# Optimization experiments

Hardware: AMD Instinct MI355X
Metric: run time of the kernel (lower is better)

Reference implementation:

```python
import math
import jax, jax.numpy as jnp
import numpy as np

NUM_HEADS = 16
HEAD_DIM = 128
BLOCK = 256
EPS = 1e-6


def _get_slopes(n):
    def p2(n):
        start = 2 ** (-2 ** (-(math.log2(n) - 3)))
        return [start * start ** i for i in range(n)]
    if math.log2(n).is_integer():
        return p2(n)
    c = 2 ** math.floor(math.log2(n))
    return p2(c) + _get_slopes(2 * c)[0::2][: n - c]


def setup_inputs() -> dict:
    key = jax.random.key(0)
    ks = jax.random.split(key, 4)
    d_in, d_out = 2048, 2048
    x = jax.random.normal(ks[0], (2, 4096, d_in), dtype=jnp.float32)
    Wqkv = jax.random.normal(ks[1], (d_in, 3 * NUM_HEADS * HEAD_DIM), dtype=jnp.float32) * 0.02
    Wg = jax.random.normal(ks[2], (d_in, NUM_HEADS * HEAD_DIM), dtype=jnp.float32) * 0.02
    Wout = jax.random.normal(ks[3], (NUM_HEADS * HEAD_DIM, d_out), dtype=jnp.float32) * 0.02
    norm_w = jnp.ones((NUM_HEADS * HEAD_DIM,), dtype=jnp.float32)
    return {"x": x, "Wqkv": Wqkv, "Wg": Wg, "Wout": Wout, "norm_w": norm_w}


def reference(x, Wqkv, Wg, Wout, norm_w):
    b, n, _ = x.shape
    h, d = NUM_HEADS, HEAD_DIM
    nb = n // BLOCK  # seq_len chosen divisible by block_size

    # slopes (ALiBi-style), shape [h,1,1]
    slope = jnp.asarray(_get_slopes(h), dtype=jnp.float32).reshape(h, 1, 1)

    qkv = jax.nn.silu(x @ Wqkv)                       # [b,n,3hd]
    qkv = qkv.reshape(b, n, h, 3 * d)
    q, k, v = jnp.split(qkv, 3, axis=-1)              # each [b,n,h,d]
    q = q.transpose(0, 2, 1, 3)                       # [b,h,n,d]
    k = k.transpose(0, 2, 1, 3)
    v = v.transpose(0, 2, 1, 3)

    # per-position decay factors within a block
    arr = jnp.arange(BLOCK, dtype=jnp.float32) + 1.0          # [B]
    q_decay = jnp.exp(-slope * arr[:, None])                  # [h,B,1]
    k_decay = jnp.exp(-slope * (BLOCK - arr[:, None]))        # [h,B,1]
    idx = arr[:, None] - arr[None, :]                         # [B,B]
    diag_decay = jnp.where(idx >= 0, jnp.exp(-slope[None] * idx[None, None]), 0.0)  # [1,h,B,B]
    block_decay = jnp.exp(-slope * BLOCK)                     # [h,1,1]

    # blocked xs: [nb, b, h, B, d]
    def to_blocks(t):
        return t.reshape(b, h, nb, BLOCK, d).transpose(2, 0, 1, 3, 4)

    qb, kb, vb = to_blocks(q), to_blocks(k), to_blocks(v)

    def step(kv, blk):
        qi, ki, vi = blk                                       # [b,h,B,d]
        # inter-block: (qi * q_decay) @ kv  -> [b,h,B,d]
        non_diag = jnp.einsum('bhmd,bhde->bhme', qi * q_decay, kv)
        # intra-block causal decayed attention
        qk = jnp.einsum('bhmd,bhnd->bhmn', qi, ki) * diag_decay
        diag = jnp.einsum('bhmn,bhne->bhme', qk, vi)
        out = non_diag + diag
        kv_new = block_decay * kv + jnp.einsum('bhmd,bhme->bhde', ki * k_decay, vi)
        return kv_new, out

    kv0 = jnp.zeros((b, h, d, d), dtype=jnp.float32)
    _, out_blocks = jax.lax.scan(step, kv0, (qb, kb, vb))      # [nb,b,h,B,d]
    o = out_blocks.transpose(1, 2, 0, 3, 4).reshape(b, h, n, d)
    o = o.transpose(0, 2, 1, 3).reshape(b, n, h * d)           # [b,n,hd]

    # T5 (RMS) LayerNorm
    var = jnp.mean(o * o, axis=-1, keepdims=True)
    o = o * jax.lax.rsqrt(var + EPS) * norm_w

    # output gate and projection
    o = jax.nn.sigmoid(x @ Wg) * o
    return o @ Wout
```

## Files before the change

kernel.cpp:

```cpp
#include <hip/hip_runtime.h>
#include <cstddef>

typedef float f32x4 __attribute__((ext_vector_type(4)));
typedef __bf16 bf16x8 __attribute__((ext_vector_type(8)));
typedef unsigned short u16x8 __attribute__((ext_vector_type(8)));
typedef unsigned short u16x4 __attribute__((ext_vector_type(4)));

constexpr int NB = 2, S = 4096, H = 16, D = 128;
constexpr int DIN = 2048, NQKV = 6144, HD = 2048;
constexpr int BLK = 256, NBL = 16;

constexpr size_t SZ_XB    = (size_t)NB * S * DIN * 2;
constexpr size_t SZ_WQKVT = (size_t)NQKV * DIN * 2;
constexpr size_t SZ_WGT   = (size_t)HD * DIN * 2;
constexpr size_t SZ_WOUTT = (size_t)HD * HD * 2;
constexpr size_t SZ_QKVB  = (size_t)NB * S * NQKV * 2;
constexpr size_t SZ_GB    = (size_t)NB * S * HD * 2;
constexpr size_t SZ_ST    = (size_t)NB * H * NBL * D * D * 2;
constexpr size_t SZ_OB    = (size_t)NB * S * HD * 2;

__device__ __forceinline__ float bf2f(unsigned short u) {
  return __uint_as_float(((unsigned)u) << 16);
}
__device__ __forceinline__ unsigned short f2bf(float f) {
  unsigned u = __float_as_uint(f);
  u += 0x7fffu + ((u >> 16) & 1u);
  return (unsigned short)(u >> 16);
}
__device__ __forceinline__ void gload16(const void* g, void* l) {
  __builtin_amdgcn_global_load_lds(
      (const __attribute__((address_space(1))) unsigned int*)g,
      (__attribute__((address_space(3))) unsigned int*)l, 16, 0, 0);
}

__global__ __launch_bounds__(256) void cvt_bf16(
    const float* __restrict__ in, unsigned short* __restrict__ out) {
  const size_t id = (size_t)blockIdx.x * 256 + threadIdx.x;
  const float4 a = *(const float4*)&in[id * 8];
  const float4 c = *(const float4*)&in[id * 8 + 4];
  u16x8 o;
  o[0] = f2bf(a.x); o[1] = f2bf(a.y); o[2] = f2bf(a.z); o[3] = f2bf(a.w);
  o[4] = f2bf(c.x); o[5] = f2bf(c.y); o[6] = f2bf(c.z); o[7] = f2bf(c.w);
  *(u16x8*)&out[id * 8] = o;
}

__global__ __launch_bounds__(256) void transpose_cvt(
    const float* __restrict__ W, unsigned short* __restrict__ Wt, int K, int N) {
  __shared__ unsigned short tile[32][33];
  const int n0 = blockIdx.x * 32, k0 = blockIdx.y * 32;
  const int t = threadIdx.x;
  const int r = t >> 3, c4 = (t & 7) * 4;
  const float4 v = *(const float4*)&W[(size_t)(k0 + r) * N + n0 + c4];
  tile[r][c4 + 0] = f2bf(v.x);
  tile[r][c4 + 1] = f2bf(v.y);
  tile[r][c4 + 2] = f2bf(v.z);
  tile[r][c4 + 3] = f2bf(v.w);
  __syncthreads();
  u16x4 o;
  #pragma unroll
  for (int i = 0; i < 4; ++i) o[i] = tile[c4 + i][r];
  *(u16x4*)&Wt[(size_t)(n0 + r) * K + k0 + c4] = o;
}

template<int ACT>
__global__ __launch_bounds__(512, 2) void gemm256(
    const unsigned short* __restrict__ A, const unsigned short* __restrict__ Bt,
    void* __restrict__ C, int M, int N, int K) {
  __shared__ unsigned short lds[65536];
  char* ldsb = (char*)lds;
  const int t = threadIdx.x;
  const int lane = t & 63, wave = t >> 6;
  const int wr = wave >> 2, wc = wave & 3;

  const int nbn = N >> 8;
  const int nwg = gridDim.x;
  int lin = blockIdx.x;
  lin = (lin & 7) * (nwg >> 3) + (lin >> 3);
  const int bm = lin / nbn, bn = lin % nbn;

  const int subr = lane >> 2;
  const int sw = (subr & 6) << 3;
  const int cstg = ((((lane & 3) << 4) ^ sw) >> 1);
  const int r0 = wave * 32 + subr;
  const unsigned short* srcA0 = A  + (size_t)(bm * 256 + r0) * K + cstg;
  const unsigned short* srcA1 = A  + (size_t)(bm * 256 + r0 + 16) * K + cstg;
  const unsigned short* srcB0 = Bt + (size_t)(bn * 256 + r0) * K + cstg;
  const unsigned short* srcB1 = Bt + (size_t)(bn * 256 + r0 + 16) * K + cstg;
  const int dst0 = wave * 2048, dst1 = dst0 + 1024;

  const int colb = (lane >> 4) << 4;
  int offA[8], offB[4];
  #pragma unroll
  for (int m = 0; m < 8; ++m) {
    const int row = wr * 128 + m * 16 + (lane & 15);
    offA[m] = ((row >> 4) << 10) + (((((row & 15) << 6) | colb)) ^ ((row & 6) << 3));
  }
  #pragma unroll
  for (int n = 0; n < 4; ++n) {
    const int row = wc * 64 + n * 16 + (lane & 15);
    offB[n] = ((row >> 4) << 10) + (((((row & 15) << 6) | colb)) ^ ((row & 6) << 3));
  }

  const int NU = K >> 5;
  #define STAGE(u) {                                                   \
    const int _s = ((u) & 3) * 32768;                                  \
    const int _ko = (u) * 32;                                          \
    gload16(srcA0 + _ko, ldsb + _s + dst0);                            \
    gload16(srcA1 + _ko, ldsb + _s + dst1);                            \
    gload16(srcB0 + _ko, ldsb + _s + 16384 + dst0);                    \
    gload16(srcB1 + _ko, ldsb + _s + 16384 + dst1);                    \
  }

  STAGE(0); STAGE(1); STAGE(2);

  f32x4 acc[8][4] = {};
  for (int u = 0; u < NU; ++u) {
    if (u < NU - 2)      asm volatile("s_waitcnt vmcnt(8)" ::: "memory");
    else if (u == NU - 2) asm volatile("s_waitcnt vmcnt(4)" ::: "memory");
    else                  asm volatile("s_waitcnt vmcnt(0)" ::: "memory");
    __builtin_amdgcn_s_barrier();
    if (u + 3 < NU) STAGE(u + 3);
    const int slot = (u & 3) * 32768;
    bf16x8 af[8], bf[4];
    #pragma unroll
    for (int m = 0; m < 8; ++m) af[m] = *(const bf16x8*)(ldsb + slot + offA[m]);
    #pragma unroll
    for (int n = 0; n < 4; ++n) bf[n] = *(const bf16x8*)(ldsb + slot + 16384 + offB[n]);
    __builtin_amdgcn_s_setprio(1);
    #pragma unroll
    for (int m = 0; m < 8; ++m)
      #pragma unroll
      for (int n = 0; n < 4; ++n)
        acc[m][n] = __builtin_amdgcn_mfma_f32_16x16x32_bf16(af[m], bf[n], acc[m][n], 0, 0, 0);
    __builtin_amdgcn_s_setprio(0);
  }
  #undef STAGE

  const int ro = (lane >> 4) * 4, co = lane & 15;
  #pragma unroll
  for (int m = 0; m < 8; ++m)
    #pragma unroll
    for (int n = 0; n < 4; ++n) {
      const int gc = bn * 256 + wc * 64 + n * 16 + co;
      #pragma unroll
      for (int r = 0; r < 4; ++r) {
        const int gr = bm * 256 + wr * 128 + m * 16 + ro + r;
        float v = acc[m][n][r];
        if constexpr (ACT == 1) v = v / (1.f + __expf(-v));
        if constexpr (ACT == 2) v = 1.f / (1.f + __expf(-v));
        if constexpr (ACT == 0) ((float*)C)[(size_t)gr * N + gc] = v;
        else ((unsigned short*)C)[(size_t)gr * N + gc] = f2bf(v);
      }
    }
}

__global__ __launch_bounds__(256) void kv_outer(
    const unsigned short* __restrict__ qkv, unsigned short* __restrict__ st) {
  const int gid = blockIdx.x;
  const int j = gid & 15;
  const int bh = gid >> 4;
  const int h = bh & 15;
  const int b = bh >> 4;
  const float slope = exp2f(-0.5f * (float)(h + 1));
  const int t = threadIdx.x;
  __shared__ unsigned short kl[64][136];
  __shared__ unsigned short vl[64][136];
  float acc[8][8] = {};
  const int e0 = (t >> 4) * 8, f0 = (t & 15) * 8;
  for (int ch = 0; ch < 4; ++ch) {
    if (ch) __syncthreads();
    #pragma unroll
    for (int i = 0; i < 4; ++i) {
      const int cc = t + 256 * i;
      const int r = cc >> 4, c0 = (cc & 15) * 8;
      const int mb = ch * 64 + r;
      const int seq = b * S + j * BLK + mb;
      const u16x8 k8 = *(const u16x8*)&qkv[(size_t)seq * NQKV + h * 384 + 128 + c0];
      const float kd = expf(-slope * (float)(255 - mb));
      u16x8 kw;
      #pragma unroll
      for (int q2 = 0; q2 < 8; ++q2) kw[q2] = f2bf(bf2f(k8[q2]) * kd);
      *(u16x8*)&kl[r][c0] = kw;
      *(u16x8*)&vl[r][c0] = *(const u16x8*)&qkv[(size_t)seq * NQKV + h * 384 + 256 + c0];
    }
    __syncthreads();
    for (int m = 0; m < 64; ++m) {
      const u16x8 k8 = *(const u16x8*)&kl[m][e0];
      const u16x8 v8 = *(const u16x8*)&vl[m][f0];
      float kf[8], vf[8];
      #pragma unroll
      for (int q2 = 0; q2 < 8; ++q2) { kf[q2] = bf2f(k8[q2]); vf[q2] = bf2f(v8[q2]); }
      #pragma unroll
      for (int i = 0; i < 8; ++i)
        #pragma unroll
        for (int q2 = 0; q2 < 8; ++q2) acc[i][q2] += kf[i] * vf[q2];
    }
  }
  const size_t base = (size_t)gid * (D * D);
  #pragma unroll
  for (int q2 = 0; q2 < 8; ++q2) {
    u16x8 ow;
    #pragma unroll
    for (int i = 0; i < 8; ++i) ow[i] = f2bf(acc[i][q2]);
    *(u16x8*)&st[base + (size_t)(f0 + q2) * D + e0] = ow;
  }
}

__global__ __launch_bounds__(256) void kv_scan(unsigned short* __restrict__ st) {
  const int id = blockIdx.x * 256 + threadIdx.x;
  const int ef = id & (D * D - 1);
  const int bh = id >> 14;
  const int h = bh & 15;
  const float slope = exp2f(-0.5f * (float)(h + 1));
  const float bd = expf(-slope * 256.f);
  unsigned short* p = st + (size_t)bh * NBL * D * D + ef;
  float cur = 0.f;
  #pragma unroll
  for (int jj = 0; jj < NBL; ++jj) {
    const float m = bf2f(p[(size_t)jj * D * D]);
    p[(size_t)jj * D * D] = f2bf(cur);
    cur = bd * cur + m;
  }
}

__global__ __launch_bounds__(256) void attn_mfma(
    const unsigned short* __restrict__ qkv, const unsigned short* __restrict__ st,
    unsigned short* __restrict__ ob) {
  const int gid = blockIdx.x;
  const int half = gid & 1;
  const int rest = gid >> 1;
  const int j = rest & 15;
  const int bh = rest >> 4;
  const int h = bh & 15;
  const int b = bh >> 4;
  const float slope = exp2f(-0.5f * (float)(h + 1));
  const int t = threadIdx.x;
  const int lane = t & 63, wave = t >> 6, wr = wave >> 1, wc = wave & 1;

  __shared__ unsigned short ql[128][136];
  __shared__ unsigned short cb[128][136];
  __shared__ unsigned short pl[128][136];

  {
    const int r = t >> 4, c0 = (t & 15) * 8;
    const size_t stbase = (size_t)rest * (D * D);
    #pragma unroll
    for (int p = 0; p < 8; ++p) {
      const int seq = b * S + j * BLK + half * 128 + r + p * 16;
      *(u16x8*)&ql[r + p * 16][c0] = *(const u16x8*)&qkv[(size_t)seq * NQKV + h * 384 + c0];
      *(u16x8*)&cb[r + p * 16][c0] = *(const u16x8*)&st[stbase + (size_t)(r + p * 16) * D + c0];
    }
  }
  __syncthreads();

  f32x4 acc[4][4] = {};
  #pragma unroll
  for (int kk = 0; kk < 4; ++kk) {
    bf16x8 af[4], bfr[4];
    #pragma unroll
    for (int m = 0; m < 4; ++m)
      af[m] = *(const bf16x8*)&ql[wr * 64 + m * 16 + (lane & 15)][kk * 32 + (lane >> 4) * 8];
    #pragma unroll
    for (int n = 0; n < 4; ++n)
      bfr[n] = *(const bf16x8*)&cb[wc * 64 + n * 16 + (lane & 15)][kk * 32 + (lane >> 4) * 8];
    #pragma unroll
    for (int m = 0; m < 4; ++m)
      #pragma unroll
      for (int n = 0; n < 4; ++n)
        acc[m][n] = __builtin_amdgcn_mfma_f32_16x16x32_bf16(af[m], bfr[n], acc[m][n], 0, 0, 0);
  }
  const int ro = (lane >> 4) * 4;
  #pragma unroll
  for (int m = 0; m < 4; ++m)
    #pragma unroll
    for (int r = 0; r < 4; ++r) {
      const int gm = half * 128 + wr * 64 + m * 16 + ro + r;
      const float qd = expf(-slope * (float)(gm + 1));
      #pragma unroll
      for (int n = 0; n < 4; ++n) acc[m][n][r] *= qd;
    }

  const int nch = 1 + half;
  for (int c = 0; c < nch; ++c) {
    __syncthreads();
    {
      const int r = t >> 4, c0 = (t & 15) * 8;
      #pragma unroll
      for (int p = 0; p < 8; ++p) {
        const int seq = b * S + j * BLK + c * 128 + r + p * 16;
        *(u16x8*)&cb[r + p * 16][c0] = *(const u16x8*)&qkv[(size_t)seq * NQKV + h * 384 + 128 + c0];
      }
    }
    __syncthreads();
    f32x4 sacc[4][4] = {};
    #pragma unroll
    for (int kk = 0; kk < 4; ++kk) {
      bf16x8 af[4], bfr[4];
      #pragma unroll
      for (int m = 0; m < 4; ++m)
        af[m] = *(const bf16x8*)&ql[wr * 64 + m * 16 + (lane & 15)][kk * 32 + (lane >> 4) * 8];
      #pragma unroll
      for (int n = 0; n < 4; ++n)
        bfr[n] = *(const bf16x8*)&cb[wc * 64 + n * 16 + (lane & 15)][kk * 32 + (lane >> 4) * 8];
      #pragma unroll
      for (int m = 0; m < 4; ++m)
        #pragma unroll
        for (int n = 0; n < 4; ++n)
          sacc[m][n] = __builtin_amdgcn_mfma_f32_16x16x32_bf16(af[m], bfr[n], sacc[m][n], 0, 0, 0);
    }
    #pragma unroll
    for (int m = 0; m < 4; ++m)
      #pragma unroll
      for (int n = 0; n < 4; ++n) {
        const int lc = wc * 64 + n * 16 + (lane & 15);
        const int gp = c * 128 + lc;
        #pragma unroll
        for (int r = 0; r < 4; ++r) {
          const int lm = wr * 64 + m * 16 + ro + r;
          const int gm = half * 128 + lm;
          const float dd = (gm >= gp) ? expf(-slope * (float)(gm - gp)) : 0.f;
          pl[lm][lc] = f2bf(sacc[m][n][r] * dd);
        }
      }
    __syncthreads();
    {
      const int vr = t & 15, vc0 = (t >> 4) * 8;
      #pragma unroll
      for (int p = 0; p < 8; ++p) {
        const int row = vr + p * 16;
        const int seq = b * S + j * BLK + c * 128 + row;
        const u16x8 vv = *(const u16x8*)&qkv[(size_t)seq * NQKV + h * 384 + 256 + vc0];
        #pragma unroll
        for (int i = 0; i < 8; ++i) cb[vc0 + i][row] = vv[i];
      }
    }
    __syncthreads();
    #pragma unroll
    for (int kk = 0; kk < 4; ++kk) {
      bf16x8 af[4], bfr[4];
      #pragma unroll
      for (int m = 0; m < 4; ++m)
        af[m] = *(const bf16x8*)&pl[wr * 64 + m * 16 + (lane & 15)][kk * 32 + (lane >> 4) * 8];
      #pragma unroll
      for (int n = 0; n < 4; ++n)
        bfr[n] = *(const bf16x8*)&cb[wc * 64 + n * 16 + (lane & 15)][kk * 32 + (lane >> 4) * 8];
      #pragma unroll
      for (int m = 0; m < 4; ++m)
        #pragma unroll
        for (int n = 0; n < 4; ++n)
          acc[m][n] = __builtin_amdgcn_mfma_f32_16x16x32_bf16(af[m], bfr[n], acc[m][n], 0, 0, 0);
    }
  }

  #pragma unroll
  for (int m = 0; m < 4; ++m)
    #pragma unroll
    for (int n = 0; n < 4; ++n) {
      const int fc = h * D + wc * 64 + n * 16 + (lane & 15);
      #pragma unroll
      for (int r = 0; r < 4; ++r) {
        const int seq = b * S + j * BLK + half * 128 + wr * 64 + m * 16 + ro + r;
        ob[(size_t)seq * HD + fc] = f2bf(acc[m][n][r]);
      }
    }
}

__global__ __launch_bounds__(256) void norm_gate(
    const unsigned short* __restrict__ ob, const unsigned short* __restrict__ gb,
    const float* __restrict__ nw, unsigned short* __restrict__ og) {
  const int row = blockIdx.x;
  const int t = threadIdx.x;
  const u16x8 ov = *(const u16x8*)&ob[(size_t)row * HD + t * 8];
  float f[8];
  float ss = 0.f;
  #pragma unroll
  for (int i = 0; i < 8; ++i) { f[i] = bf2f(ov[i]); ss += f[i] * f[i]; }
  #pragma unroll
  for (int off = 32; off > 0; off >>= 1) ss += __shfl_down(ss, off, 64);
  __shared__ float red[4];
  if ((t & 63) == 0) red[t >> 6] = ss;
  __syncthreads();
  const float rms = rsqrtf((red[0] + red[1] + red[2] + red[3]) * (1.f / HD) + 1e-6f);
  const u16x8 gv = *(const u16x8*)&gb[(size_t)row * HD + t * 8];
  u16x8 ow;
  #pragma unroll
  for (int i = 0; i < 8; ++i)
    ow[i] = f2bf(f[i] * rms * nw[t * 8 + i] * bf2f(gv[i]));
  *(u16x8*)&og[(size_t)row * HD + t * 8] = ow;
}

extern "C" void kernel_launch(void* const* d_in, const int* in_sizes, int n_in,
                              void* d_out, int out_size, void* d_ws, size_t ws_size,
                              hipStream_t stream) {
  (void)in_sizes; (void)n_in; (void)out_size; (void)ws_size;
  const float* x    = (const float*)d_in[0];
  const float* Wqkv = (const float*)d_in[1];
  const float* Wg   = (const float*)d_in[2];
  const float* Wout = (const float*)d_in[3];
  const float* nw   = (const float*)d_in[4];

  char* ws = (char*)d_ws;
  unsigned short* xb    = (unsigned short*)ws; ws += SZ_XB;
  unsigned short* wqkvt = (unsigned short*)ws; ws += SZ_WQKVT;
  unsigned short* wgt   = (unsigned short*)ws; ws += SZ_WGT;
  unsigned short* woutt = (unsigned short*)ws; ws += SZ_WOUTT;
  unsigned short* qkvb  = (unsigned short*)ws; ws += SZ_QKVB;
  unsigned short* gb    = (unsigned short*)ws; ws += SZ_GB;
  unsigned short* st    = (unsigned short*)ws; ws += SZ_ST;
  unsigned short* ob    = (unsigned short*)ws; ws += SZ_OB;
  unsigned short* og    = xb;

  cvt_bf16<<<dim3((NB * S * DIN) / (256 * 8)), 256, 0, stream>>>(x, xb);
  transpose_cvt<<<dim3(NQKV / 32, DIN / 32), 256, 0, stream>>>(Wqkv, wqkvt, DIN, NQKV);
  transpose_cvt<<<dim3(HD / 32, DIN / 32), 256, 0, stream>>>(Wg, wgt, DIN, HD);
  transpose_cvt<<<dim3(HD / 32, HD / 32), 256, 0, stream>>>(Wout, woutt, HD, HD);

  gemm256<1><<<dim3((NB * S / 256) * (NQKV / 256)), 512, 0, stream>>>(xb, wqkvt, qkvb, NB * S, NQKV, DIN);
  gemm256<2><<<dim3((NB * S / 256) * (HD / 256)), 512, 0, stream>>>(xb, wgt, gb, NB * S, HD, DIN);

  kv_outer<<<dim3(NB * H * NBL), 256, 0, stream>>>(qkvb, st);
  kv_scan<<<dim3((NB * H * D * D) / 256), 256, 0, stream>>>(st);
  attn_mfma<<<dim3(NB * H * NBL * 2), 256, 0, stream>>>(qkvb, st, ob);

  norm_gate<<<dim3(NB * S), 256, 0, stream>>>(ob, gb, nw, og);
  gemm256<0><<<dim3((NB * S / 256) * (HD / 256)), 512, 0, stream>>>(og, woutt, d_out, NB * S, HD, HD);
}
```

Measured before the change: 532.4 us.

## Split GEMM main loop into two MFMA phases with interleaved A/B staging

Restructures the 256x256 bf16 GEMM main loop so each K-step runs in two halves. Each half loads part of the A fragments from LDS, issues the global-to-LDS prefetch for A or B separately, and runs 16 MFMAs, with barriers between halves. It also switches to a simpler row-major LDS layout with an XOR swizzle on the low row bits, and to an XCD-aware block mapping that groups M tiles per XCD. The aim is finer-grained overlap of LDS reads, global loads and MFMA, plus better L2 locality, at the cost of more barriers per iteration and a swizzle that may cause more LDS bank conflicts.

```diff
diff --git a/kernel.cpp b/kernel.cpp
--- a/kernel.cpp
+++ b/kernel.cpp
@@ -72,69 +72,80 @@
   const int lane = t & 63, wave = t >> 6;
   const int wr = wave >> 2, wc = wave & 3;
 
-  const int nbn = N >> 8;
-  const int nwg = gridDim.x;
-  int lin = blockIdx.x;
-  lin = (lin & 7) * (nwg >> 3) + (lin >> 3);
-  const int bm = lin / nbn, bn = lin % nbn;
-
-  const int subr = lane >> 2;
-  const int sw = (subr & 6) << 3;
-  const int cstg = ((((lane & 3) << 4) ^ sw) >> 1);
-  const int r0 = wave * 32 + subr;
-  const unsigned short* srcA0 = A  + (size_t)(bm * 256 + r0) * K + cstg;
-  const unsigned short* srcA1 = A  + (size_t)(bm * 256 + r0 + 16) * K + cstg;
-  const unsigned short* srcB0 = Bt + (size_t)(bn * 256 + r0) * K + cstg;
-  const unsigned short* srcB1 = Bt + (size_t)(bn * 256 + r0 + 16) * K + cstg;
-  const int dst0 = wave * 2048, dst1 = dst0 + 1024;
-
-  const int colb = (lane >> 4) << 4;
+  const int nbm = M >> 8, nbn = N >> 8;
+  const int nbmx = nbm >> 3;
+  const int xcd = blockIdx.x & 7, q = blockIdx.x >> 3;
+  const int bm = xcd * nbmx + (q % nbmx);
+  const int bn = q / nbmx;
+
+  const int lrow = lane >> 2;
+  const int lcg  = (lane & 3) ^ (lrow & 3);
+  const unsigned short* sA0 = A  + (size_t)(bm * 256 + wave * 32 + lrow) * K + lcg * 8;
+  const unsigned short* sA1 = A  + (size_t)(bm * 256 + wave * 32 + 16 + lrow) * K + lcg * 8;
+  const unsigned short* sB0 = Bt + (size_t)(bn * 256 + wave * 32 + lrow) * K + lcg * 8;
+  const unsigned short* sB1 = Bt + (size_t)(bn * 256 + wave * 32 + 16 + lrow) * K + lcg * 8;
+  const int dA0 = wave * 2048, dA1 = wave * 2048 + 1024;
+  const int dB0 = 16384 + dA0, dB1 = 16384 + dA1;
+
+  const int cgb = (lane >> 4) << 4;
   int offA[8], offB[4];
   #pragma unroll
   for (int m = 0; m < 8; ++m) {
     const int row = wr * 128 + m * 16 + (lane & 15);
-    offA[m] = ((row >> 4) << 10) + (((((row & 15) << 6) | colb)) ^ ((row & 6) << 3));
+    offA[m] = row * 64 + (cgb ^ ((row & 3) << 4));
   }
   #pragma unroll
   for (int n = 0; n < 4; ++n) {
     const int row = wc * 64 + n * 16 + (lane & 15);
-    offB[n] = ((row >> 4) << 10) + (((((row & 15) << 6) | colb)) ^ ((row & 6) << 3));
-  }
-
-  const int NU = K >> 5;
-  #define STAGE(u) {                                                   \
-    const int _s = ((u) & 3) * 32768;                                  \
-    const int _ko = (u) * 32;                                          \
-    gload16(srcA0 + _ko, ldsb + _s + dst0);                            \
-    gload16(srcA1 + _ko, ldsb + _s + dst1);                            \
-    gload16(srcB0 + _ko, ldsb + _s + 16384 + dst0);                    \
-    gload16(srcB1 + _ko, ldsb + _s + 16384 + dst1);                    \
-  }
-
-  STAGE(0); STAGE(1); STAGE(2);
+    offB[n] = 16384 + row * 64 + (cgb ^ ((row & 3) << 4));
+  }
+
+  const int NT = K >> 5;
+  #define STG_A(u) { const int _s = ((u) & 3) * 32768; const int _o = (u) * 32; \
+    gload16(sA0 + _o, ldsb + _s + dA0); gload16(sA1 + _o, ldsb + _s + dA1); }
+  #define STG_B(u) { const int _s = ((u) & 3) * 32768; const int _o = (u) * 32; \
+    gload16(sB0 + _o, ldsb + _s + dB0); gload16(sB1 + _o, ldsb + _s + dB1); }
+
+  STG_A(0); STG_B(0); STG_A(1); STG_B(1); STG_A(2); STG_B(2);
+  asm volatile("s_waitcnt vmcnt(8)" ::: "memory");
+  __builtin_amdgcn_s_barrier();
 
   f32x4 acc[8][4] = {};
-  for (int u = 0; u < NU; ++u) {
-    if (u < NU - 2)      asm volatile("s_waitcnt vmcnt(8)" ::: "memory");
-    else if (u == NU - 2) asm volatile("s_waitcnt vmcnt(4)" ::: "memory");
-    else                  asm volatile("s_waitcnt vmcnt(0)" ::: "memory");
+  for (int u = 0; u < NT; ++u) {
+    const int slot = (u & 3) * 32768;
+    bf16x8 af[4], bf[4];
+    #pragma unroll
+    for (int n = 0; n < 4; ++n) bf[n] = *(const bf16x8*)(ldsb + slot + offB[n]);
+    #pragma unroll
+    for (int m = 0; m < 4; ++m) af[m] = *(const bf16x8*)(ldsb + slot + offA[m]);
+    if (u + 3 < NT) STG_A(u + 3);
     __builtin_amdgcn_s_barrier();
-    if (u + 3 < NU) STAGE(u + 3);
-    const int slot = (u & 3) * 32768;
-    bf16x8 af[8], bf[4];
-    #pragma unroll
-    for (int m = 0; m < 8; ++m) af[m] = *(const bf16x8*)(ldsb + slot + offA[m]);
-    #pragma unroll
-    for (int n = 0; n < 4; ++n) bf[n] = *(const bf16x8*)(ldsb + slot + 16384 + offB[n]);
     __builtin_amdgcn_s_setprio(1);
     #pragma unroll
-    for (int m = 0; m < 8; ++m)
+    for (int m = 0; m < 4; ++m)
       #pragma unroll
       for (int n = 0; n < 4; ++n)
         acc[m][n] = __builtin_amdgcn_mfma_f32_16x16x32_bf16(af[m], bf[n], acc[m][n], 0, 0, 0);
     __builtin_amdgcn_s_setprio(0);
-  }
-  #undef STAGE
+    __builtin_amdgcn_s_barrier();
+    #pragma unroll
+    for (int m = 0; m < 4; ++m) af[m] = *(const bf16x8*)(ldsb + slot + offA[4 + m]);
+    if (u + 3 < NT) STG_B(u + 3);
+    if (u < NT - 3)       asm volatile("s_waitcnt vmcnt(8)" ::: "memory");
+    else if (u == NT - 3) asm volatile("s_waitcnt vmcnt(4)" ::: "memory");
+    else                  asm volatile("s_waitcnt vmcnt(0)" ::: "memory");
+    __builtin_amdgcn_s_barrier();
+    __builtin_amdgcn_s_setprio(1);
+    #pragma unroll
+    for (int m = 0; m < 4; ++m)
+      #pragma unroll
+      for (int n = 0; n < 4; ++n)
+        acc[4 + m][n] = __builtin_amdgcn_mfma_f32_16x16x32_bf16(af[m], bf[n], acc[4 + m][n], 0, 0, 0);
+    __builtin_amdgcn_s_setprio(0);
+    __builtin_amdgcn_s_barrier();
+  }
+  #undef STG_A
+  #undef STG_B
 
   const int ro = (lane >> 4) * 4, co = lane & 15;
   #pragma unroll
```

Result: slower. 546.8 us (+2.7%).
